# Kernel tuning notes

Hardware: AMD Instinct MI355X
Metric: run time of the kernel (lower is better)

## Reference

```python
import jax, jax.numpy as jnp
import numpy as np
import math

C_Z, C_HID, N_HEADS = 128, 32, 4
B, N = 1, 320
LN_EPS = 1e-5


def setup_inputs() -> dict:
    key = jax.random.key(0)
    ks = jax.random.split(key, 9)
    d = C_HID * N_HEADS  # 128
    glorot = math.sqrt(2.0 / (C_Z + d))
    return {
        "z": jax.random.normal(ks[0], (B, N, N, C_Z), jnp.float32),
        "mask_bias": jax.random.normal(ks[1], (B, N, 1, 1, N), jnp.float32),
        "edge_bias": jax.random.normal(ks[2], (B, 1, N_HEADS, N, N), jnp.float32),
        "wq": jax.random.normal(ks[3], (d, C_Z), jnp.float32) * glorot,
        "wk": jax.random.normal(ks[4], (d, C_Z), jnp.float32) * glorot,
        "wv": jax.random.normal(ks[5], (d, C_Z), jnp.float32) * glorot,
        "wg": jax.random.normal(ks[6], (d, C_Z), jnp.float32) * 0.02,
        "wo": jax.random.normal(ks[7], (C_Z, d), jnp.float32) * 0.02,
        "ln_w": jnp.ones((C_Z,), jnp.float32),
        "ln_b": jnp.zeros((C_Z,), jnp.float32),
    }


def reference(z, mask_bias, edge_bias, wq, wk, wv, wg, wo, ln_w, ln_b):
    # LayerNorm over c_z
    mu = jnp.mean(z, axis=-1, keepdims=True)
    var = jnp.mean(jnp.square(z - mu), axis=-1, keepdims=True)
    zn = (z - mu) * jax.lax.rsqrt(var + LN_EPS) * ln_w + ln_b  # [B,I,J,c_z]

    def proj(w):
        p = jnp.einsum("bijd,ed->bije", zn, w)  # [B,I,J,H*c]
        p = p.reshape(zn.shape[:-1] + (N_HEADS, C_HID))  # [B,I,J,H,c]
        return jnp.swapaxes(p, -3, -2)  # [B,I,H,J,c]

    q = proj(wq) / math.sqrt(C_HID)
    k = proj(wk)
    v = proj(wv)

    # scores: [B,I,H,Q,K] + mask_bias [B,I,1,1,K] + edge_bias [B,1,H,Q,K]
    scores = jnp.einsum("bihqc,bihkc->bihqk", q, k) + mask_bias + edge_bias
    a = jax.nn.softmax(scores, axis=-1)
    o = jnp.einsum("bihqk,bihkc->bihqc", a, v)  # [B,I,H,J,c]
    o = jnp.swapaxes(o, -3, -2)  # [B,I,J,H,c]

    g = jax.nn.sigmoid(jnp.einsum("bijd,ed->bije", zn, wg))
    g = g.reshape(zn.shape[:-1] + (N_HEADS, C_HID))
    o = o * g

    o = o.reshape(o.shape[:-2] + (N_HEADS * C_HID,))  # [B,I,J,H*c]
    return jnp.einsum("bije,de->bijd", o, wo)  # [B,I,J,c_z]
```

## Files before the change

kernel.cpp:

```cpp
#include <hip/hip_runtime.h>
#include <hip/hip_bf16.h>

#define NRES 320
#define CZ 128
#define NH 4
#define CH 32
#define DM 128
#define NPOS (NRES*NRES)
#define LN_EPS 1e-5f
#define QSCALE 0.17677669529663687f
#define LOG2E 1.4426950408889634f

using bf16 = __hip_bfloat16;
typedef _Float16 half_t;
typedef __attribute__((ext_vector_type(8))) _Float16 half8;
typedef __attribute__((ext_vector_type(8))) short short8;
typedef __attribute__((ext_vector_type(4))) float floatx4;

__device__ __forceinline__ float bflo(uint32_t u){ return __uint_as_float(u << 16); }
__device__ __forceinline__ float bfhi(uint32_t u){ return __uint_as_float(u & 0xffff0000u); }
__device__ __forceinline__ bf16 tob(float f){ return __float2bfloat16(f); }
__device__ __forceinline__ uint32_t cvtpk(float a, float b){
    uint32_t r;
    asm("v_cvt_pk_bf16_f32 %0, %1, %2" : "=v"(r) : "v"(a), "v"(b));
    return r;
}
__device__ __forceinline__ uint32_t cvtpkh(float a, float b){
    uint32_t r;
    asm("v_cvt_pkrtz_f16_f32 %0, %1, %2" : "=v"(r) : "v"(a), "v"(b));
    return r;
}
__device__ __forceinline__ float h2f_lo(uint32_t u){
    const half_t h = *(const half_t*)&u;
    return (float)h;
}
__device__ __forceinline__ float h2f_hi(uint32_t u){
    const uint32_t s = u >> 16;
    const half_t h = *(const half_t*)&s;
    return (float)h;
}

__global__ __launch_bounds__(256)
void k_packall(const float* __restrict__ wq, const float* __restrict__ wk,
               const float* __restrict__ wv, const float* __restrict__ wg,
               const float* __restrict__ wo, const float* __restrict__ eb,
               const float* __restrict__ mb,
               half_t* __restrict__ Apk, half_t* __restrict__ B2,
               bf16* __restrict__ ebpk, float* __restrict__ mbpk)
{
    const int idx = blockIdx.x * 256 + threadIdx.x;
    if (idx < 65536) {
        const int j = idx & 7, lane = (idx >> 3) & 63;
        const int ks = (idx >> 9) & 3, mf = (idx >> 11) & 3, wid = idx >> 13;
        const int e = wid*64 + mf*16 + (lane & 15);
        const int k = ks*32 + (lane >> 4)*8 + j;
        const float* w = (e >> 7) == 0 ? wq : (e >> 7) == 1 ? wk : (e >> 7) == 2 ? wv : wg;
        float wv_ = w[(e & 127)*CZ + k];
        if (e < 128) wv_ *= QSCALE * LOG2E;
        Apk[idx] = (half_t)wv_;
    } else if (idx < 81920) {
        const int id = idx - 65536;
        const int j = id & 7, lane = (id >> 3) & 63;
        const int nr = (id >> 9) & 3, ks = (id >> 11) & 3, wn = id >> 13;
        const int n = wn*64 + nr*16 + (lane & 15);
        const int k = ks*32 + ((lane >> 4) << 3) + j;
        B2[id] = (half_t)wo[n*DM + k];
    } else if (idx < 491520) {
        const int id = idx - 81920;
        const int e = id & 7;
        const int lane = (id >> 3) & 63;
        const int f = (id >> 9) % 20;
        const int t = (id / 10240) % 10;
        const int h = id / 102400;
        const int q = f*16 + (lane & 15);
        const int k = t*32 + (e >> 2)*16 + (lane >> 4)*4 + (e & 3);
        ebpk[id] = tob(eb[((size_t)h*NRES + q)*NRES + k] * LOG2E);
    } else {
        const int id = idx - 491520;
        mbpk[id] = mb[id] * LOG2E;
    }
}

__global__ __launch_bounds__(512, 3)
void k_lnproj(const float* __restrict__ z, const float* __restrict__ ln_w,
              const float* __restrict__ ln_b, const half_t* __restrict__ Apk,
              bf16* __restrict__ qws, bf16* __restrict__ kws,
              bf16* __restrict__ vtws, half_t* __restrict__ gows)
{
    __shared__ __align__(16) char Bs[16 * 1040];
    const int tid = threadIdx.x;
    const int p0 = blockIdx.x * 64;
    const int lane = tid & 63, wid = tid >> 6;
    const int l15 = lane & 15, g = lane >> 4;

    {
        const int r = tid >> 3, t = tid & 7, c0 = t*16;
        const float* zp = z + (size_t)(p0 + r)*CZ + c0;
        float v[16];
        {
            float4 t0 = *(const float4*)(zp + 0);
            float4 t1 = *(const float4*)(zp + 4);
            float4 t2 = *(const float4*)(zp + 8);
            float4 t3 = *(const float4*)(zp + 12);
            v[0]=t0.x; v[1]=t0.y; v[2]=t0.z; v[3]=t0.w;
            v[4]=t1.x; v[5]=t1.y; v[6]=t1.z; v[7]=t1.w;
            v[8]=t2.x; v[9]=t2.y; v[10]=t2.z; v[11]=t2.w;
            v[12]=t3.x; v[13]=t3.y; v[14]=t3.z; v[15]=t3.w;
        }
        float s = 0.f, s2 = 0.f;
        #pragma unroll
        for (int c = 0; c < 16; ++c) { s += v[c]; s2 = fmaf(v[c], v[c], s2); }
        s  += __shfl_xor(s, 1);  s  += __shfl_xor(s, 2);  s  += __shfl_xor(s, 4);
        s2 += __shfl_xor(s2, 1); s2 += __shfl_xor(s2, 2); s2 += __shfl_xor(s2, 4);
        const float mu = s * 0.0078125f;
        const float rs = rsqrtf(s2 * 0.0078125f - mu*mu + LN_EPS);
        uint32_t hd[8];
        #pragma unroll
        for (int c2 = 0; c2 < 8; ++c2) {
            const float v0 = (v[2*c2]   - mu) * rs * ln_w[c0 + 2*c2]   + ln_b[c0 + 2*c2];
            const float v1 = (v[2*c2+1] - mu) * rs * ln_w[c0 + 2*c2+1] + ln_b[c0 + 2*c2+1];
            hd[c2] = cvtpkh(v0, v1);
        }
        *(uint4*)(Bs + (2*t    )*1040 + r*16) = make_uint4(hd[0], hd[1], hd[2], hd[3]);
        *(uint4*)(Bs + (2*t + 1)*1040 + r*16) = make_uint4(hd[4], hd[5], hd[6], hd[7]);
    }
    __syncthreads();

    floatx4 acc[4][4];
    #pragma unroll
    for (int mf = 0; mf < 4; ++mf)
        #pragma unroll
        for (int nf = 0; nf < 4; ++nf)
            acc[mf][nf] = (floatx4){0.f, 0.f, 0.f, 0.f};

    const uint4* ap = (const uint4*)Apk;
    #pragma unroll
    for (int ks = 0; ks < 4; ++ks) {
        uint4 ahv[4];
        #pragma unroll
        for (int mf = 0; mf < 4; ++mf)
            ahv[mf] = ap[((wid*4 + mf)*4 + ks)*64 + lane];
        #pragma unroll
        for (int nf = 0; nf < 4; ++nf) {
            const int off = (ks*4 + g)*1040 + (16*nf + l15)*16;
            const half8 bh = *(const half8*)(Bs + off);
            #pragma unroll
            for (int mf = 0; mf < 4; ++mf) {
                const half8 ah = *(const half8*)&ahv[mf];
                acc[mf][nf] = __builtin_amdgcn_mfma_f32_16x16x32_f16(ah, bh, acc[mf][nf], 0, 0, 0);
            }
        }
    }

    const int i = p0 / NRES;
    const int j0 = p0 % NRES;
    #pragma unroll
    for (int mf = 0; mf < 4; ++mf) {
        const int e0 = wid*64 + mf*16 + 4*g;
        const int hh = (e0 >> 5) & 3, c0 = e0 & 31;
        #pragma unroll
        for (int nf = 0; nf < 4; ++nf) {
            const int jl = nf*16 + l15;
            const floatx4 a = acc[mf][nf];
            if (wid < 4) {
                uint2 dw;
                dw.x = cvtpk(a[0], a[1]);
                dw.y = cvtpk(a[2], a[3]);
                bf16* dst = (wid < 2) ? qws : kws;
                const size_t hidx = ((size_t)((i*NH + hh)*NRES) + (j0 + jl))*CH + c0;
                *(uint2*)(dst + hidx) = dw;
            } else if (wid < 6) {
                const size_t vbase = ((size_t)((i*NH + hh)*CH) + c0)*NRES + (j0 + jl);
                vtws[vbase         ] = tob(a[0]);
                vtws[vbase +   NRES] = tob(a[1]);
                vtws[vbase + 2*NRES] = tob(a[2]);
                vtws[vbase + 3*NRES] = tob(a[3]);
            } else {
                const float g0 = 1.f / (1.f + __expf(-a[0]));
                const float g1 = 1.f / (1.f + __expf(-a[1]));
                const float g2 = 1.f / (1.f + __expf(-a[2]));
                const float g3 = 1.f / (1.f + __expf(-a[3]));
                uint2 dw;
                dw.x = cvtpkh(g0, g1);
                dw.y = cvtpkh(g2, g3);
                *(uint2*)(gows + (size_t)(p0 + jl)*DM + (e0 & 127)) = dw;
            }
        }
    }
}

__global__ __launch_bounds__(640)
void k_attn(const bf16* __restrict__ qws, const bf16* __restrict__ kws,
            const bf16* __restrict__ vtws, half_t* __restrict__ gows,
            const float* __restrict__ mbpk, const bf16* __restrict__ ebpk)
{
    __shared__ __align__(16) char psmem[10 * 32 * 80];
    const int i = blockIdx.x, h = blockIdx.y;
    const int tid = threadIdx.x;
    const int lane = tid & 63, w = tid >> 6;
    const int l15 = lane & 15, g = lane >> 4;
    const size_t slab = (size_t)(i*NH + h) * NRES * CH;
    char* psb = psmem + w*2560;

    const uint4* qg = (const uint4*)(qws + slab);
    const uint4* kg = (const uint4*)(kws + slab);
    const uint4* vg = (const uint4*)(vtws + slab);
    const float* mbr = mbpk + (size_t)i*NRES;
    const uint4* ebp = (const uint4*)ebpk;
    const int ebbase = h*12800 + w*128 + lane;

    const uint32_t onep = (l15 == 0) ? 0x3F803F80u : 0u;
    uint4 au = make_uint4(onep, onep, onep, onep);
    const short8 av2 = *(short8*)&au;

    short8 bq[2];
    #pragma unroll
    for (int nf = 0; nf < 2; ++nf) {
        uint4 t = qg[(32*w + 16*nf + l15)*4 + g];
        bq[nf] = *(short8*)&t;
    }
    uint4 kc0 = kg[(     l15)*4 + g];
    uint4 kc1 = kg[(16 + l15)*4 + g];
    uint4 ebc[2];
    #pragma unroll
    for (int nf = 0; nf < 2; ++nf) ebc[nf] = ebp[ebbase + nf*64];
    float2 mbc[2][2];
    #pragma unroll
    for (int mi = 0; mi < 2; ++mi)
        #pragma unroll
        for (int rp = 0; rp < 2; ++rp)
            mbc[mi][rp] = *(const float2*)(mbr + 16*mi + 4*g + 2*rp);

    floatx4 o[2][2];
    floatx4 o2[2];
    #pragma unroll
    for (int nf = 0; nf < 2; ++nf) {
        o[0][nf] = (floatx4){0.f, 0.f, 0.f, 0.f};
        o[1][nf] = (floatx4){0.f, 0.f, 0.f, 0.f};
        o2[nf]   = (floatx4){0.f, 0.f, 0.f, 0.f};
    }

    for (int t = 0; t < 10; ++t) {
        const int tn = (t < 9) ? t + 1 : 9;
        uint4 kn0 = kg[(32*tn +      l15)*4 + g];
        uint4 kn1 = kg[(32*tn + 16 + l15)*4 + g];
        uint4 ebn[2];
        #pragma unroll
        for (int nf = 0; nf < 2; ++nf) ebn[nf] = ebp[ebbase + tn*1280 + nf*64];
        float2 mbn[2][2];
        #pragma unroll
        for (int mi = 0; mi < 2; ++mi)
            #pragma unroll
            for (int rp = 0; rp < 2; ++rp)
                mbn[mi][rp] = *(const float2*)(mbr + 32*tn + 16*mi + 4*g + 2*rp);
        uint4 av0u = vg[(     l15)*40 + 4*t + g];
        uint4 av1u = vg[(16 + l15)*40 + 4*t + g];

        const short8 ak0 = *(short8*)&kc0;
        const short8 ak1 = *(short8*)&kc1;
        floatx4 sa[2][2];
        __builtin_amdgcn_s_setprio(1);
        #pragma unroll
        for (int nf = 0; nf < 2; ++nf) {
            const uint4 E = ebc[nf];
            const floatx4 c0 = (floatx4){bflo(E.x) + mbc[0][0].x, bfhi(E.x) + mbc[0][0].y,
                                         bflo(E.y) + mbc[0][1].x, bfhi(E.y) + mbc[0][1].y};
            const floatx4 c1 = (floatx4){bflo(E.z) + mbc[1][0].x, bfhi(E.z) + mbc[1][0].y,
                                         bflo(E.w) + mbc[1][1].x, bfhi(E.w) + mbc[1][1].y};
            sa[0][nf] = __builtin_amdgcn_mfma_f32_16x16x32_bf16(ak0, bq[nf], c0, 0, 0, 0);
            sa[1][nf] = __builtin_amdgcn_mfma_f32_16x16x32_bf16(ak1, bq[nf], c1, 0, 0, 0);
        }
        __builtin_amdgcn_s_setprio(0);

        #pragma unroll
        for (int nf = 0; nf < 2; ++nf) {
            const int qrow = 16*nf + l15;
            #pragma unroll
            for (int mi = 0; mi < 2; ++mi) {
                const float p0 = exp2f(sa[mi][nf][0]);
                const float p1 = exp2f(sa[mi][nf][1]);
                const float p2 = exp2f(sa[mi][nf][2]);
                const float p3 = exp2f(sa[mi][nf][3]);
                *(uint2*)(psb + qrow*80 + 32*mi + 8*g) =
                    make_uint2(cvtpk(p0, p1), cvtpk(p2, p3));
            }
        }
        const short8 av0 = *(short8*)&av0u;
        const short8 av1 = *(short8*)&av1u;
        __builtin_amdgcn_s_setprio(1);
        #pragma unroll
        for (int nf = 0; nf < 2; ++nf) {
            const short8 bp = *(const short8*)(psb + (16*nf + l15)*80 + 16*g);
            o[0][nf] = __builtin_amdgcn_mfma_f32_16x16x32_bf16(av0, bp, o[0][nf], 0, 0, 0);
            o[1][nf] = __builtin_amdgcn_mfma_f32_16x16x32_bf16(av1, bp, o[1][nf], 0, 0, 0);
            o2[nf]   = __builtin_amdgcn_mfma_f32_16x16x32_bf16(av2, bp, o2[nf],   0, 0, 0);
        }
        __builtin_amdgcn_s_setprio(0);
        kc0 = kn0; kc1 = kn1;
        #pragma unroll
        for (int nf = 0; nf < 2; ++nf) ebc[nf] = ebn[nf];
        #pragma unroll
        for (int mi = 0; mi < 2; ++mi)
            #pragma unroll
            for (int rp = 0; rp < 2; ++rp)
                mbc[mi][rp] = mbn[mi][rp];
    }

    float linv[2];
    #pragma unroll
    for (int nf = 0; nf < 2; ++nf) {
        const float ls = __shfl(o2[nf][0], l15);
        linv[nf] = 1.f / ls;
    }
    uint32_t* gp = (uint32_t*)gows;
    #pragma unroll
    for (int nf = 0; nf < 2; ++nf) {
        const int jq = 32*w + 16*nf + l15;
        #pragma unroll
        for (int ma = 0; ma < 2; ++ma)
            #pragma unroll
            for (int rp = 0; rp < 2; ++rp) {
                const size_t idx = ((size_t)(i*NRES + jq))*64 + h*16 + 8*ma + 2*g + rp;
                const uint32_t u = gp[idx];
                const float v0 = o[ma][nf][2*rp    ] * linv[nf] * h2f_lo(u);
                const float v1 = o[ma][nf][2*rp + 1] * linv[nf] * h2f_hi(u);
                gp[idx] = cvtpkh(v0, v1);
            }
    }
}

__global__ __launch_bounds__(512)
void k_outproj(const half_t* __restrict__ gows, const half_t* __restrict__ B2,
               float* __restrict__ out)
{
    __shared__ __align__(16) char As[16 * 4112];
    const int tid = threadIdx.x;
    const int p0 = blockIdx.x * 256;
    const int lane = tid & 63, wid = tid >> 6;
    const int wm = wid >> 1, wn = wid & 1;

    half8 bh[4][4];
    {
        const uint4* bp = (const uint4*)B2;
        #pragma unroll
        for (int ks = 0; ks < 4; ++ks)
            #pragma unroll
            for (int nr = 0; nr < 4; ++nr) {
                uint4 t = bp[(((wn*4 + ks)*4) + nr)*64 + lane];
                bh[ks][nr] = *(half8*)&t;
            }
    }

    {
        const uint4* src = (const uint4*)(gows + (size_t)p0 * DM);
        #pragma unroll
        for (int it = 0; it < 8; ++it) {
            const int t = tid + it*512;
            uint4 u = src[t];
            *(uint4*)(As + (t & 15)*4112 + (t >> 4)*16) = u;
        }
    }
    __syncthreads();

    floatx4 acc[4][4];
    #pragma unroll
    for (int m = 0; m < 4; ++m)
        #pragma unroll
        for (int n = 0; n < 4; ++n)
            acc[m][n] = (floatx4){0.f, 0.f, 0.f, 0.f};

    #pragma unroll
    for (int ks = 0; ks < 4; ++ks) {
        half8 a[4];
        #pragma unroll
        for (int m = 0; m < 4; ++m) {
            const int row = wm*64 + m*16 + (lane & 15);
            a[m] = *(const half8*)(As + (ks*4 + (lane >> 4))*4112 + row*16);
        }
        #pragma unroll
        for (int nr = 0; nr < 4; ++nr)
            #pragma unroll
            for (int m = 0; m < 4; ++m)
                acc[m][nr] = __builtin_amdgcn_mfma_f32_16x16x32_f16(a[m], bh[ks][nr], acc[m][nr], 0, 0, 0);
    }

    #pragma unroll
    for (int m = 0; m < 4; ++m) {
        #pragma unroll
        for (int n = 0; n < 4; ++n) {
            const int d = wn*64 + n*16 + (lane & 15);
            #pragma unroll
            for (int r = 0; r < 4; ++r) {
                const int prow = p0 + wm*64 + m*16 + ((lane >> 4) << 2) + r;
                out[(size_t)prow*DM + d] = acc[m][n][r];
            }
        }
    }
}

extern "C" void kernel_launch(void* const* d_in, const int* in_sizes, int n_in,
                              void* d_out, int out_size, void* d_ws, size_t ws_size,
                              hipStream_t stream)
{
    const float* z   = (const float*)d_in[0];
    const float* mb  = (const float*)d_in[1];
    const float* eb  = (const float*)d_in[2];
    const float* wq  = (const float*)d_in[3];
    const float* wk  = (const float*)d_in[4];
    const float* wv  = (const float*)d_in[5];
    const float* wg  = (const float*)d_in[6];
    const float* wo  = (const float*)d_in[7];
    const float* lnw = (const float*)d_in[8];
    const float* lnb = (const float*)d_in[9];
    float* out = (float*)d_out;

    const size_t SEG = (size_t)NPOS * DM;
    bf16* qws   = (bf16*)d_ws;
    bf16* kws   = qws + SEG;
    bf16* vtws  = kws + SEG;
    half_t* gows = (half_t*)(vtws + SEG);
    half_t* Apk  = gows + SEG;
    half_t* B2   = Apk + 65536;
    bf16* ebpk  = (bf16*)(B2 + 16384);
    float* mbpk = (float*)(ebpk + 409600);

    k_packall<<<2320, 256, 0, stream>>>(wq, wk, wv, wg, wo, eb, mb,
                                        Apk, B2, ebpk, mbpk);
    k_lnproj<<<NPOS/64, 512, 0, stream>>>(z, lnw, lnb, Apk, qws, kws, vtws, gows);
    k_attn<<<dim3(NRES, NH), 640, 0, stream>>>(qws, kws, vtws, gows, mbpk, ebpk);
    k_outproj<<<NPOS/256, 512, 0, stream>>>(gows, B2, out);
}
```

Before: 135.2 us.

## Software-pipeline attention loop with two-deep prefetch and next-tile QK overlap

Restructures the key-tile loop into a ping-pong pipeline. The QK MFMA for tile t+1 is issued after the PV MFMA of tile t, so the exp/softmax stage overlaps with matrix work. K, edge bias and mask bias are prefetched two tiles ahead and V one tile ahead using double-buffered register sets. This hides global load latency better, at the cost of more registers, which could reduce occupancy.

Result: no change. 134.9 us (-0.2%).

```diff
diff --git a/kernel.cpp b/kernel.cpp
--- a/kernel.cpp
+++ b/kernel.cpp
@@ -219,17 +219,6 @@
         uint4 t = qg[(32*w + 16*nf + l15)*4 + g];
         bq[nf] = *(short8*)&t;
     }
-    uint4 kc0 = kg[(     l15)*4 + g];
-    uint4 kc1 = kg[(16 + l15)*4 + g];
-    uint4 ebc[2];
-    #pragma unroll
-    for (int nf = 0; nf < 2; ++nf) ebc[nf] = ebp[ebbase + nf*64];
-    float2 mbc[2][2];
-    #pragma unroll
-    for (int mi = 0; mi < 2; ++mi)
-        #pragma unroll
-        for (int rp = 0; rp < 2; ++rp)
-            mbc[mi][rp] = *(const float2*)(mbr + 16*mi + 4*g + 2*rp);
 
     floatx4 o[2][2];
     floatx4 o2[2];
@@ -239,72 +228,117 @@
         o[1][nf] = (floatx4){0.f, 0.f, 0.f, 0.f};
         o2[nf]   = (floatx4){0.f, 0.f, 0.f, 0.f};
     }
-
-    for (int t = 0; t < 10; ++t) {
-        const int tn = (t < 9) ? t + 1 : 9;
-        uint4 kn0 = kg[(32*tn +      l15)*4 + g];
-        uint4 kn1 = kg[(32*tn + 16 + l15)*4 + g];
-        uint4 ebn[2];
-        #pragma unroll
-        for (int nf = 0; nf < 2; ++nf) ebn[nf] = ebp[ebbase + tn*1280 + nf*64];
-        float2 mbn[2][2];
-        #pragma unroll
-        for (int mi = 0; mi < 2; ++mi)
-            #pragma unroll
-            for (int rp = 0; rp < 2; ++rp)
-                mbn[mi][rp] = *(const float2*)(mbr + 32*tn + 16*mi + 4*g + 2*rp);
-        uint4 av0u = vg[(     l15)*40 + 4*t + g];
-        uint4 av1u = vg[(16 + l15)*40 + 4*t + g];
-
-        const short8 ak0 = *(short8*)&kc0;
-        const short8 ak1 = *(short8*)&kc1;
-        floatx4 sa[2][2];
-        __builtin_amdgcn_s_setprio(1);
+    floatx4 sa[2][2];
+
+    uint4 kA0, kA1, kB0, kB1;
+    uint4 ebA[2], ebB[2];
+    float2 mbA[2][2], mbB[2][2];
+    uint4 vA0, vA1, vB0, vB1;
+
+    kA0 = kg[(     l15)*4 + g];
+    kA1 = kg[(16 + l15)*4 + g];
+    #pragma unroll
+    for (int nf = 0; nf < 2; ++nf) ebA[nf] = ebp[ebbase + nf*64];
+    #pragma unroll
+    for (int mi = 0; mi < 2; ++mi)
+        #pragma unroll
+        for (int rp = 0; rp < 2; ++rp)
+            mbA[mi][rp] = *(const float2*)(mbr + 16*mi + 4*g + 2*rp);
+    {
+        const short8 a0 = *(short8*)&kA0;
+        const short8 a1 = *(short8*)&kA1;
         #pragma unroll
         for (int nf = 0; nf < 2; ++nf) {
-            const uint4 E = ebc[nf];
-            const floatx4 c0 = (floatx4){bflo(E.x) + mbc[0][0].x, bfhi(E.x) + mbc[0][0].y,
-                                         bflo(E.y) + mbc[0][1].x, bfhi(E.y) + mbc[0][1].y};
-            const floatx4 c1 = (floatx4){bflo(E.z) + mbc[1][0].x, bfhi(E.z) + mbc[1][0].y,
-                                         bflo(E.w) + mbc[1][1].x, bfhi(E.w) + mbc[1][1].y};
-            sa[0][nf] = __builtin_amdgcn_mfma_f32_16x16x32_bf16(ak0, bq[nf], c0, 0, 0, 0);
-            sa[1][nf] = __builtin_amdgcn_mfma_f32_16x16x32_bf16(ak1, bq[nf], c1, 0, 0, 0);
-        }
-        __builtin_amdgcn_s_setprio(0);
-
-        #pragma unroll
-        for (int nf = 0; nf < 2; ++nf) {
-            const int qrow = 16*nf + l15;
-            #pragma unroll
-            for (int mi = 0; mi < 2; ++mi) {
-                const float p0 = exp2f(sa[mi][nf][0]);
-                const float p1 = exp2f(sa[mi][nf][1]);
-                const float p2 = exp2f(sa[mi][nf][2]);
-                const float p3 = exp2f(sa[mi][nf][3]);
-                *(uint2*)(psb + qrow*80 + 32*mi + 8*g) =
-                    make_uint2(cvtpk(p0, p1), cvtpk(p2, p3));
-            }
-        }
-        const short8 av0 = *(short8*)&av0u;
-        const short8 av1 = *(short8*)&av1u;
-        __builtin_amdgcn_s_setprio(1);
-        #pragma unroll
-        for (int nf = 0; nf < 2; ++nf) {
-            const short8 bp = *(const short8*)(psb + (16*nf + l15)*80 + 16*g);
-            o[0][nf] = __builtin_amdgcn_mfma_f32_16x16x32_bf16(av0, bp, o[0][nf], 0, 0, 0);
-            o[1][nf] = __builtin_amdgcn_mfma_f32_16x16x32_bf16(av1, bp, o[1][nf], 0, 0, 0);
-            o2[nf]   = __builtin_amdgcn_mfma_f32_16x16x32_bf16(av2, bp, o2[nf],   0, 0, 0);
-        }
-        __builtin_amdgcn_s_setprio(0);
-        kc0 = kn0; kc1 = kn1;
-        #pragma unroll
-        for (int nf = 0; nf < 2; ++nf) ebc[nf] = ebn[nf];
-        #pragma unroll
-        for (int mi = 0; mi < 2; ++mi)
-            #pragma unroll
-            for (int rp = 0; rp < 2; ++rp)
-                mbc[mi][rp] = mbn[mi][rp];
-    }
+            const uint4 E = ebA[nf];
+            const floatx4 c0 = (floatx4){bflo(E.x) + mbA[0][0].x, bfhi(E.x) + mbA[0][0].y,
+                                         bflo(E.y) + mbA[0][1].x, bfhi(E.y) + mbA[0][1].y};
+            const floatx4 c1 = (floatx4){bflo(E.z) + mbA[1][0].x, bfhi(E.z) + mbA[1][0].y,
+                                         bflo(E.w) + mbA[1][1].x, bfhi(E.w) + mbA[1][1].y};
+            sa[0][nf] = __builtin_amdgcn_mfma_f32_16x16x32_bf16(a0, bq[nf], c0, 0, 0, 0);
+            sa[1][nf] = __builtin_amdgcn_mfma_f32_16x16x32_bf16(a1, bq[nf], c1, 0, 0, 0);
+        }
+    }
+    kB0 = kg[(32 +      l15)*4 + g];
+    kB1 = kg[(32 + 16 + l15)*4 + g];
+    #pragma unroll
+    for (int nf = 0; nf < 2; ++nf) ebB[nf] = ebp[ebbase + 1280 + nf*64];
+    #pragma unroll
+    for (int mi = 0; mi < 2; ++mi)
+        #pragma unroll
+        for (int rp = 0; rp < 2; ++rp)
+            mbB[mi][rp] = *(const float2*)(mbr + 32 + 16*mi + 4*g + 2*rp);
+    vA0 = vg[(     l15)*40 + g];
+    vA1 = vg[(16 + l15)*40 + g];
+
+#define ATTN_BODY(T, KU0, KU1, EBU, MBU, VU0, VU1, KL0, KL1, EBL, MBL, VL0, VL1)   \
+    {                                                                              \
+        const int tn1 = ((T) < 9) ? (T) + 1 : 9;                                   \
+        const int tn2 = ((T) < 8) ? (T) + 2 : 9;                                   \
+        KL0 = kg[(32*tn2 +      l15)*4 + g];                                       \
+        KL1 = kg[(32*tn2 + 16 + l15)*4 + g];                                       \
+        _Pragma("unroll")                                                          \
+        for (int nf = 0; nf < 2; ++nf) EBL[nf] = ebp[ebbase + tn2*1280 + nf*64];   \
+        _Pragma("unroll")                                                          \
+        for (int mi = 0; mi < 2; ++mi)                                             \
+            _Pragma("unroll")                                                      \
+            for (int rp = 0; rp < 2; ++rp)                                         \
+                MBL[mi][rp] = *(const float2*)(mbr + 32*tn2 + 16*mi + 4*g + 2*rp); \
+        VL0 = vg[(     l15)*40 + 4*tn1 + g];                                       \
+        VL1 = vg[(16 + l15)*40 + 4*tn1 + g];                                       \
+                                             \
+        _Pragma("unroll")                                                          \
+        for (int nf = 0; nf < 2; ++nf) {                                           \
+            const int qrow = 16*nf + l15;                                          \
+            _Pragma("unroll")                                                      \
+            for (int mi = 0; mi < 2; ++mi) {                                       \
+                const float p0 = exp2f(sa[mi][nf][0]);                             \
+                const float p1 = exp2f(sa[mi][nf][1]);                             \
+                const float p2 = exp2f(sa[mi][nf][2]);                             \
+                const float p3 = exp2f(sa[mi][nf][3]);                             \
+                *(uint2*)(psb + qrow*80 + 32*mi + 8*g) =                           \
+                    make_uint2(cvtpk(p0, p1), cvtpk(p2, p3));                      \
+            }                                                                      \
+        }                                                                          \
+                                                                       \
+        {                                                                          \
+            const short8 av0 = *(short8*)&VU0;                                     \
+            const short8 av1 = *(short8*)&VU1;                                     \
+            __builtin_amdgcn_s_setprio(1);                                         \
+            _Pragma("unroll")                                                      \
+            for (int nf = 0; nf < 2; ++nf) {                                       \
+                const short8 bp = *(const short8*)(psb + (16*nf + l15)*80 + 16*g); \
+                o[0][nf] = __builtin_amdgcn_mfma_f32_16x16x32_bf16(av0, bp, o[0][nf], 0, 0, 0); \
+                o[1][nf] = __builtin_amdgcn_mfma_f32_16x16x32_bf16(av1, bp, o[1][nf], 0, 0, 0); \
+                o2[nf]   = __builtin_amdgcn_mfma_f32_16x16x32_bf16(av2, bp, o2[nf],   0, 0, 0); \
+            }                                                                      \
+            __builtin_amdgcn_s_setprio(0);                                         \
+        }                                                                          \
+                       \
+        {                                                                          \
+            const short8 a0 = *(short8*)&KU0;                                      \
+            const short8 a1 = *(short8*)&KU1;                                      \
+            __builtin_amdgcn_s_setprio(1);                                         \
+            _Pragma("unroll")                                                      \
+            for (int nf = 0; nf < 2; ++nf) {                                       \
+                const uint4 E = EBU[nf];                                           \
+                const floatx4 c0 = (floatx4){bflo(E.x) + MBU[0][0].x, bfhi(E.x) + MBU[0][0].y, \
+                                             bflo(E.y) + MBU[0][1].x, bfhi(E.y) + MBU[0][1].y}; \
+                const floatx4 c1 = (floatx4){bflo(E.z) + MBU[1][0].x, bfhi(E.z) + MBU[1][0].y, \
+                                             bflo(E.w) + MBU[1][1].x, bfhi(E.w) + MBU[1][1].y}; \
+                sa[0][nf] = __builtin_amdgcn_mfma_f32_16x16x32_bf16(a0, bq[nf], c0, 0, 0, 0); \
+                sa[1][nf] = __builtin_amdgcn_mfma_f32_16x16x32_bf16(a1, bq[nf], c1, 0, 0, 0); \
+            }                                                                      \
+            __builtin_amdgcn_s_setprio(0);                                         \
+        }                                                                          \
+    }
+
+    for (int tp = 0; tp < 5; ++tp) {
+        ATTN_BODY(2*tp,     kB0, kB1, ebB, mbB, vA0, vA1,
+                            kA0, kA1, ebA, mbA, vB0, vB1)
+        ATTN_BODY(2*tp + 1, kA0, kA1, ebA, mbA, vB0, vB1,
+                            kB0, kB1, ebB, mbB, vA0, vA1)
+    }
+#undef ATTN_BODY
 
     float linv[2];
     #pragma unroll
```
